# Performance work log

Measured on AMD Instinct MI355X. Metric: run time of the kernel, lower is better.

The kernel has to match this reference:

```python
import jax, jax.numpy as jnp
import numpy as np

G = 64          # graphs in batch
P = 31          # original nodes per graph
N_ORIG = G * P  # 1984 original nodes
N = N_ORIG + G  # 2048 total nodes (one virtual node per graph, appended at end)
D = 512         # hidden_dim
H = 8           # num_heads
DK = D // H     # per-head dim
FF = 2048       # dim_ff
L = 4           # num_layers
NF = 32         # num_node_features
MAX_SP = 100
MAX_DEG = 100


def setup_inputs() -> dict:
    key = jax.random.key(0)
    ks = jax.random.split(key, 24)
    s = 0.02
    return {
        "x": jax.random.normal(ks[0], (N_ORIG, NF), jnp.float32),
        "sp_matrix": jax.random.randint(ks[1], (N_ORIG, N_ORIG), 0, MAX_SP + 1, jnp.int32),
        "batch_ids": jnp.concatenate([
            jnp.repeat(jnp.arange(G, dtype=jnp.int32), P),
            jnp.arange(G, dtype=jnp.int32),
        ]),
        "degrees": jax.random.randint(ks[2], (N,), 0, MAX_DEG + 1, jnp.int32),
        "init_W": jax.random.normal(ks[3], (NF, D), jnp.float32) * s,
        "init_b": jnp.zeros((D,), jnp.float32),
        "cent_emb": jax.random.normal(ks[4], (MAX_DEG + 1, D), jnp.float32) * s,
        "dist_biases": jax.random.normal(ks[5], (MAX_SP + 2,), jnp.float32) * s,
        "virt_bias": jnp.zeros((), jnp.float32),
        "Wq": jax.random.normal(ks[6], (L, H, D, DK), jnp.float32) * s,
        "bq": jnp.zeros((L, H, DK), jnp.float32),
        "Wk": jax.random.normal(ks[7], (L, H, D, DK), jnp.float32) * s,
        "bk": jnp.zeros((L, H, DK), jnp.float32),
        "Wv": jax.random.normal(ks[8], (L, H, D, DK), jnp.float32) * s,
        "bv": jnp.zeros((L, H, DK), jnp.float32),
        "Wo": jax.random.normal(ks[9], (L, D, D), jnp.float32) * s,
        "bo": jnp.zeros((L, D), jnp.float32),
        "W1": jax.random.normal(ks[10], (L, D, FF), jnp.float32) * s,
        "b1": jnp.zeros((L, FF), jnp.float32),
        "W2": jax.random.normal(ks[11], (L, FF, D), jnp.float32) * s,
        "b2": jnp.zeros((L, D), jnp.float32),
    }


def _ln(h):
    # F.layer_norm with no affine params, eps=1e-5
    m = jnp.mean(h, axis=-1, keepdims=True)
    v = jnp.var(h, axis=-1, keepdims=True)
    return (h - m) / jnp.sqrt(v + 1e-5)


def reference(x, sp_matrix, batch_ids, degrees,
              init_W, init_b, cent_emb, dist_biases, virt_bias,
              Wq, bq, Wk, bk, Wv, bv, Wo, bo, W1, b1, W2, b2):
    same = batch_ids[:, None] == batch_ids[None, :]          # attention mask [N, N]
    is_virt = jnp.arange(N) >= N_ORIG

    # B matrix: fill with last distance bias (detached: torch uses .item()),
    # overwrite orig-orig block with sp-distance biases, virtual edges with
    # virt_bias, diagonal with dist_biases[0].
    fill = jax.lax.stop_gradient(dist_biases[-1])
    B = jnp.full((N, N), fill, dtype=jnp.float32)
    sp = jnp.minimum(sp_matrix, MAX_SP)
    B = B.at[:N_ORIG, :N_ORIG].set(dist_biases[sp])
    ve = (is_virt[:, None] ^ is_virt[None, :]) & same        # virt<->non-virt, same graph
    B = jnp.where(ve, virt_bias, B)
    diag = jnp.arange(N)
    B = B.at[diag, diag].set(dist_biases[0])

    # init projection, append virtual node states, add centrality encoding
    h = x @ init_W + init_b                                  # [N_ORIG, D]
    h = jnp.concatenate([h, jnp.zeros((G, D), h.dtype)], axis=0)   # [N, D]
    h = h + cent_emb[jnp.minimum(degrees, MAX_DEG)]

    scale = 1.0 / jnp.sqrt(jnp.float32(DK))
    for l in range(L):
        hn = _ln(h)
        Q = jnp.einsum('nd,hdk->hnk', hn, Wq[l]) + bq[l][:, None, :]   # [H, N, DK]
        K = jnp.einsum('nd,hdk->hnk', hn, Wk[l]) + bk[l][:, None, :]
        V = jnp.einsum('nd,hdk->hnk', hn, Wv[l]) + bv[l][:, None, :]
        logits = jnp.einsum('hik,hjk->hij', Q, K) * scale + B          # [H, N, N]
        logits = jnp.where(same, logits, -jnp.inf)
        w = jax.nn.softmax(logits, axis=-1)
        o = jnp.einsum('hij,hjk->hik', w, V)                           # [H, N, DK]
        o = jnp.transpose(o, (1, 0, 2)).reshape(N, D)                  # concat heads
        h = o @ Wo[l] + bo[l] + h                                      # residual
        hn2 = _ln(h)
        h = h + jax.nn.relu(hn2 @ W1[l] + b1[l]) @ W2[l] + b2[l]       # FFN residual

    return h[N_ORIG:]   # virtual node states, [G, D]
```

## Files before the change

kernel.cpp:

```cpp
#include <hip/hip_runtime.h>


#define NG   64
#define NP   31
#define NORI 1984
#define NT   2048
#define DIM  512
#define NHD  8
#define DKH  64
#define FFD  2048
#define NLAY 4
#define NFEA 32

typedef __attribute__((ext_vector_type(8))) short short8;
typedef __attribute__((ext_vector_type(4))) float floatx4;

__device__ __forceinline__ unsigned short f2bf(float f) {
    union { float f; unsigned u; } v; v.f = f;
    unsigned r = v.u + 0x7fffu + ((v.u >> 16) & 1u);
    return (unsigned short)(r >> 16);
}
__device__ __forceinline__ float bf2f(unsigned short u) {
    union { unsigned u; float f; } v; v.u = ((unsigned)u) << 16;
    return v.f;
}

__global__ __launch_bounds__(256) void build_B(
    const int* __restrict__ sp, const float* __restrict__ db,
    const float* __restrict__ virt_bias, float* __restrict__ Bg)
{
    int g = blockIdx.x;
    float vb = virt_bias[0];
    for (int e = threadIdx.x; e < 1024; e += 256) {
        int i = e >> 5, j = e & 31;
        float v;
        if (i == j) v = db[0];
        else if (i < NP && j < NP) {
            int s = sp[(size_t)(g * NP + i) * NORI + g * NP + j];
            v = db[s < 100 ? s : 100];
        } else v = vb;
        Bg[(size_t)g * 1024 + e] = v;
    }
}

__global__ __launch_bounds__(256) void init_h(
    const float* __restrict__ x, const int* __restrict__ degrees,
    const float* __restrict__ init_W, const float* __restrict__ init_b,
    const float* __restrict__ cent_emb, float* __restrict__ h)
{
    int n = blockIdx.x;
    int tid = threadIdx.x;
    __shared__ float xs[NFEA];
    if (n < NORI && tid < NFEA) xs[tid] = x[(size_t)n * NFEA + tid];
    __syncthreads();
    int deg = degrees[n]; if (deg > 100) deg = 100;
    for (int d = tid; d < DIM; d += 256) {
        float v = cent_emb[(size_t)deg * DIM + d];
        if (n < NORI) {
            float acc = init_b[d];
            #pragma unroll
            for (int k = 0; k < NFEA; ++k) acc += xs[k] * init_W[(size_t)k * DIM + d];
            v += acc;
        }
        h[(size_t)n * DIM + d] = v;
    }
}

__global__ __launch_bounds__(256) void qkv_prep(
    const float* __restrict__ Wq, const float* __restrict__ Wk, const float* __restrict__ Wv,
    unsigned short* __restrict__ Wt)
{
    int tile = blockIdx.x;
    int slice = tile >> 5;
    int tloc = tile & 31;
    int dt = tloc >> 1, kt = tloc & 1;
    int l = slice / 24; int rem = slice % 24; int which = rem >> 3; int hh = rem & 7;
    const float* W = (which == 0) ? Wq : (which == 1) ? Wk : Wv;
    const float* in = W + (size_t)(l * 8 + hh) * DIM * DKH;
    __shared__ float tl[32][33];
    int tr = threadIdx.x >> 5, tc = threadIdx.x & 31;
    #pragma unroll
    for (int p = 0; p < 4; ++p)
        tl[tr + p * 8][tc] = in[(size_t)(dt * 32 + tr + p * 8) * DKH + kt * 32 + tc];
    __syncthreads();
    unsigned short* out = Wt + ((size_t)l * 1536 + which * 512 + hh * 64 + kt * 32) * DIM + dt * 32;
    #pragma unroll
    for (int p = 0; p < 4; ++p)
        out[(size_t)(tr + p * 8) * DIM + tc] = f2bf(tl[tc][tr + p * 8]);
}

__global__ __launch_bounds__(256) void bias_prep(
    const float* __restrict__ bq, const float* __restrict__ bk, const float* __restrict__ bv,
    float* __restrict__ bqkv)
{
    int idx = blockIdx.x * 256 + threadIdx.x;
    if (idx >= NLAY * 1536) return;
    int l = idx / 1536, c = idx % 1536;
    int which = c >> 9, cc = c & 511;
    const float* b = (which == 0) ? bq : (which == 1) ? bk : bv;
    bqkv[idx] = b[(size_t)l * 512 + cc];
}

__global__ __launch_bounds__(256) void prep_w(
    const float* __restrict__ Wo, const float* __restrict__ W1, const float* __restrict__ W2,
    unsigned short* __restrict__ Wo_t, unsigned short* __restrict__ W1_t,
    unsigned short* __restrict__ W2_t)
{
    int id = blockIdx.x;
    const float* in; unsigned short* out; int R, C, l, rt, ct;
    if (id < 1024) {
        l = id >> 8; int t = id & 255; rt = t >> 4; ct = t & 15;
        in = Wo; out = Wo_t; R = 512; C = 512;
    } else if (id < 5120) {
        int t2 = id - 1024; l = t2 >> 10; int t = t2 & 1023; rt = t >> 6; ct = t & 63;
        in = W1; out = W1_t; R = 512; C = 2048;
    } else {
        int t2 = id - 5120; l = t2 >> 10; int t = t2 & 1023; rt = t >> 4; ct = t & 15;
        in = W2; out = W2_t; R = 2048; C = 512;
    }
    const float* ip = in + (size_t)l * R * C;
    unsigned short* op = out + (size_t)l * R * C;
    int r0 = rt * 32, c0 = ct * 32;
    __shared__ float tl[32][33];
    int tr = threadIdx.x >> 5, tc = threadIdx.x & 31;
    #pragma unroll
    for (int p = 0; p < 4; ++p)
        tl[tr + p * 8][tc] = ip[(size_t)(r0 + tr + p * 8) * C + c0 + tc];
    __syncthreads();
    #pragma unroll
    for (int p = 0; p < 4; ++p)
        op[(size_t)(c0 + tr + p * 8) * R + r0 + tc] = f2bf(tl[tc][tr + p * 8]);
}

__global__ __launch_bounds__(256) void layernorm_bf16(
    const float* __restrict__ in, unsigned short* __restrict__ out, int row0)
{
    int n = row0 + blockIdx.x;
    int tid = threadIdx.x;
    const float* row = in + (size_t)n * DIM;
    float v0 = row[tid], v1 = row[tid + 256];
    float s = v0 + v1;
    float sq = v0 * v0 + v1 * v1;
    #pragma unroll
    for (int off = 32; off > 0; off >>= 1) {
        s  += __shfl_down(s, off);
        sq += __shfl_down(sq, off);
    }
    __shared__ float red[8];
    int wave = tid >> 6;
    if ((tid & 63) == 0) { red[wave] = s; red[4 + wave] = sq; }
    __syncthreads();
    float ts  = red[0] + red[1] + red[2] + red[3];
    float tsq = red[4] + red[5] + red[6] + red[7];
    float m   = ts * (1.0f / DIM);
    float var = tsq * (1.0f / DIM) - m * m;
    float inv = rsqrtf(var + 1e-5f);
    out[(size_t)n * DIM + tid]       = f2bf((v0 - m) * inv);
    out[(size_t)n * DIM + tid + 256] = f2bf((v1 - m) * inv);
}

template<int SPLITK>
__global__ __launch_bounds__(256) void gemm_bf16(
    const unsigned short* __restrict__ A, const unsigned short* __restrict__ Bt,
    const float* __restrict__ bias, void* __restrict__ out,
    int Nfull, int K, int moff, int noff, int flags)
{
    __shared__ __align__(16) unsigned short Asl[64 * 72];
    __shared__ __align__(16) unsigned short Bsl[64 * 72];
    int tid = threadIdx.x;
    int row0 = moff + blockIdx.y * 64, col0 = noff + blockIdx.x * 64;
    if ((flags & 4) && col0 < 512 && row0 < NORI) return;
    int kslice = K / SPLITK;
    int kbeg = blockIdx.z * kslice;
    int wave = tid >> 6, lane = tid & 63;
    int quad = lane >> 4, m16 = lane & 15;
    int mw = (wave >> 1) * 32, nw = (wave & 1) * 32;
    floatx4 acc[2][2] = {};
    for (int k0 = kbeg; k0 < kbeg + kslice; k0 += 64) {
        #pragma unroll
        for (int p = 0; p < 2; ++p) {
            int idx = (p * 256 + tid) * 8;
            int r = idx >> 6, kk = idx & 63;
            *(float4*)(Asl + r * 72 + kk) =
                *(const float4*)(A + (size_t)(row0 + r) * K + k0 + kk);
            *(float4*)(Bsl + r * 72 + kk) =
                *(const float4*)(Bt + (size_t)(col0 + r) * K + k0 + kk);
        }
        __syncthreads();
        #pragma unroll
        for (int ks = 0; ks < 64; ks += 32) {
            short8 a[2], b[2];
            #pragma unroll
            for (int mi = 0; mi < 2; ++mi)
                a[mi] = *(const short8*)(Asl + (mw + mi * 16 + m16) * 72 + ks + quad * 8);
            #pragma unroll
            for (int ni = 0; ni < 2; ++ni)
                b[ni] = *(const short8*)(Bsl + (nw + ni * 16 + m16) * 72 + ks + quad * 8);
            #pragma unroll
            for (int mi = 0; mi < 2; ++mi)
                #pragma unroll
                for (int ni = 0; ni < 2; ++ni)
                    acc[mi][ni] = __builtin_amdgcn_mfma_f32_16x16x32_bf16(
                        a[mi], b[ni], acc[mi][ni], 0, 0, 0);
        }
        __syncthreads();
    }
    if (SPLITK == 1) {
        int do_relu = flags & 1, out_bf = flags & 2;
        #pragma unroll
        for (int mi = 0; mi < 2; ++mi) {
            #pragma unroll
            for (int ni = 0; ni < 2; ++ni) {
                int col = col0 + nw + ni * 16 + m16;
                float bval = bias ? bias[col] : 0.0f;
                #pragma unroll
                for (int rr = 0; rr < 4; ++rr) {
                    int row = row0 + mw + mi * 16 + quad * 4 + rr;
                    float v = acc[mi][ni][rr] + bval;
                    if (do_relu) v = fmaxf(v, 0.0f);
                    if (out_bf) ((unsigned short*)out)[(size_t)row * Nfull + col] = f2bf(v);
                    else        ((float*)out)[(size_t)row * Nfull + col] = v;
                }
            }
        }
    } else {
        float* o = (float*)out;
        float bscale = (blockIdx.z == 0) ? 1.0f : 0.0f;
        #pragma unroll
        for (int mi = 0; mi < 2; ++mi) {
            #pragma unroll
            for (int ni = 0; ni < 2; ++ni) {
                int col = col0 + nw + ni * 16 + m16;
                float bval = bias[col] * bscale;
                #pragma unroll
                for (int rr = 0; rr < 4; ++rr) {
                    int row = row0 + mw + mi * 16 + quad * 4 + rr;
                    atomicAdd(&o[(size_t)row * Nfull + col], acc[mi][ni][rr] + bval);
                }
            }
        }
    }
}

__global__ __launch_bounds__(256) void attention(
    const unsigned short* __restrict__ qkv,
    const float* __restrict__ Bg,
    unsigned short* __restrict__ O)
{
    int g = blockIdx.x >> 3;
    int hh = blockIdx.x & 7;
    __shared__ float Qs[32][65], Ks[32][65], Vs[32][65];
    __shared__ float S[32][33];
    int tid = threadIdx.x;
    int i = tid >> 3;
    int c0 = (tid & 7) * 8;
    int gn = (i < NP) ? g * NP + i : NORI + g;
    const unsigned short* base = qkv + (size_t)gn * 1536 + hh * DKH;
    short8 qv = *(const short8*)(base + c0);
    short8 kv = *(const short8*)(base + 512 + c0);
    short8 vv = *(const short8*)(base + 1024 + c0);
    #pragma unroll
    for (int j = 0; j < 8; ++j) {
        Qs[i][c0 + j] = bf2f((unsigned short)qv[j]);
        Ks[i][c0 + j] = bf2f((unsigned short)kv[j]);
        Vs[i][c0 + j] = bf2f((unsigned short)vv[j]);
    }
    __syncthreads();
    const float scale = 0.125f;
    #pragma unroll
    for (int e = 0; e < 4; ++e) {
        int idx = tid + e * 256;
        int si = idx >> 5, sj = idx & 31;
        float dot = 0.0f;
        #pragma unroll
        for (int k = 0; k < DKH; ++k) dot += Qs[si][k] * Ks[sj][k];
        S[si][sj] = dot * scale + Bg[(size_t)g * 1024 + si * 32 + sj];
    }
    __syncthreads();
    if (tid < 32) {
        float mx = -1e30f;
        #pragma unroll
        for (int j = 0; j < 32; ++j) mx = fmaxf(mx, S[tid][j]);
        float sum = 0.0f;
        #pragma unroll
        for (int j = 0; j < 32; ++j) { float e = __expf(S[tid][j] - mx); S[tid][j] = e; sum += e; }
        float inv = 1.0f / sum;
        #pragma unroll
        for (int j = 0; j < 32; ++j) S[tid][j] *= inv;
    }
    __syncthreads();
    short8 ov;
    #pragma unroll
    for (int cc = 0; cc < 8; ++cc) {
        float acc = 0.0f;
        #pragma unroll
        for (int j = 0; j < 32; ++j) acc += S[i][j] * Vs[j][c0 + cc];
        ov[cc] = (short)f2bf(acc);
    }
    *(short8*)(O + (size_t)gn * DIM + hh * DKH + c0) = ov;
}

__global__ __launch_bounds__(64) void attention_last(
    const unsigned short* __restrict__ qkv, const float* __restrict__ Bg,
    unsigned short* __restrict__ O)
{
    int g = blockIdx.x >> 3, hh = blockIdx.x & 7;
    __shared__ float Ks[32][65], Vs[32][65];
    __shared__ float Qs[64], P[32];
    int tid = threadIdx.x;
    int j = tid & 31, hf = tid >> 5;
    int gn = (j < NP) ? g * NP + j : NORI + g;
    const unsigned short* kb = qkv + (size_t)gn * 1536 + hh * DKH + 512 + hf * 32;
    #pragma unroll
    for (int c = 0; c < 32; c += 8) {
        short8 k8 = *(const short8*)(kb + c);
        short8 v8 = *(const short8*)(kb + 512 + c);
        #pragma unroll
        for (int t = 0; t < 8; ++t) {
            Ks[j][hf * 32 + c + t] = bf2f((unsigned short)k8[t]);
            Vs[j][hf * 32 + c + t] = bf2f((unsigned short)v8[t]);
        }
    }
    Qs[tid] = bf2f(qkv[(size_t)(NORI + g) * 1536 + hh * DKH + tid]);
    __syncthreads();
    float s;
    if (tid < 32) {
        float dot = 0.0f;
        #pragma unroll
        for (int k = 0; k < 64; ++k) dot += Qs[k] * Ks[tid][k];
        s = dot * 0.125f + Bg[(size_t)g * 1024 + 31 * 32 + tid];
    } else s = -1e30f;
    float mx = s;
    #pragma unroll
    for (int off = 32; off > 0; off >>= 1) mx = fmaxf(mx, __shfl_xor(mx, off));
    float e = (tid < 32) ? __expf(s - mx) : 0.0f;
    float sum = e;
    #pragma unroll
    for (int off = 32; off > 0; off >>= 1) sum += __shfl_xor(sum, off);
    if (tid < 32) P[tid] = e / sum;
    __syncthreads();
    float acc = 0.0f;
    #pragma unroll
    for (int jj = 0; jj < 32; ++jj) acc += P[jj] * Vs[jj][tid];
    O[(size_t)(NORI + g) * DIM + hh * DKH + tid] = f2bf(acc);
}

extern "C" void kernel_launch(void* const* d_in, const int* in_sizes, int n_in,
                              void* d_out, int out_size, void* d_ws, size_t ws_size,
                              hipStream_t stream)
{
    const float* x        = (const float*)d_in[0];
    const int*   sp       = (const int*)d_in[1];
    const int*   degrees  = (const int*)d_in[3];
    const float* init_W   = (const float*)d_in[4];
    const float* init_b   = (const float*)d_in[5];
    const float* cent_emb = (const float*)d_in[6];
    const float* db       = (const float*)d_in[7];
    const float* vbias    = (const float*)d_in[8];
    const float* Wq       = (const float*)d_in[9];
    const float* bq       = (const float*)d_in[10];
    const float* Wk       = (const float*)d_in[11];
    const float* bk       = (const float*)d_in[12];
    const float* Wv       = (const float*)d_in[13];
    const float* bv       = (const float*)d_in[14];
    const float* Wo       = (const float*)d_in[15];
    const float* bo       = (const float*)d_in[16];
    const float* W1       = (const float*)d_in[17];
    const float* b1       = (const float*)d_in[18];
    const float* W2       = (const float*)d_in[19];
    const float* b2       = (const float*)d_in[20];

    char* ws = (char*)d_ws;
    float*          h      = (float*)ws;          ws += (size_t)NT * DIM * 4;
    unsigned short* hn     = (unsigned short*)ws; ws += (size_t)NT * DIM * 2;
    unsigned short* o      = (unsigned short*)ws; ws += (size_t)NT * DIM * 2;
    unsigned short* qkv    = (unsigned short*)ws; ws += (size_t)NT * FFD * 2;
    float*          Bg     = (float*)ws;          ws += (size_t)NG * 1024 * 4;
    unsigned short* Wqkv_t = (unsigned short*)ws; ws += (size_t)NLAY * 1536 * DIM * 2;
    unsigned short* Wo_t   = (unsigned short*)ws; ws += (size_t)NLAY * DIM * DIM * 2;
    unsigned short* W1_t   = (unsigned short*)ws; ws += (size_t)NLAY * FFD * DIM * 2;
    unsigned short* W2_t   = (unsigned short*)ws; ws += (size_t)NLAY * DIM * FFD * 2;
    float*          bqkv   = (float*)ws;          ws += (size_t)NLAY * 1536 * 4;
    unsigned short* ffnb   = qkv;

    build_B<<<NG, 256, 0, stream>>>(sp, db, vbias, Bg);
    init_h<<<NT, 256, 0, stream>>>(x, degrees, init_W, init_b, cent_emb, h);
    qkv_prep<<<96 * 32, 256, 0, stream>>>(Wq, Wk, Wv, Wqkv_t);
    bias_prep<<<(NLAY * 1536 + 255) / 256, 256, 0, stream>>>(bq, bk, bv, bqkv);
    prep_w<<<9216, 256, 0, stream>>>(Wo, W1, W2, Wo_t, W1_t, W2_t);

    for (int l = 0; l < NLAY - 1; ++l) {
        layernorm_bf16<<<NT, 256, 0, stream>>>(h, hn, 0);
        gemm_bf16<1><<<dim3(1536 / 64, NT / 64), 256, 0, stream>>>(
            hn, Wqkv_t + (size_t)l * 1536 * DIM, bqkv + (size_t)l * 1536,
            qkv, 1536, DIM, 0, 0, 2);
        attention<<<NG * NHD, 256, 0, stream>>>(qkv, Bg, o);
        gemm_bf16<2><<<dim3(DIM / 64, NT / 64, 2), 256, 0, stream>>>(
            o, Wo_t + (size_t)l * DIM * DIM, bo + (size_t)l * DIM,
            h, DIM, DIM, 0, 0, 0);
        layernorm_bf16<<<NT, 256, 0, stream>>>(h, hn, 0);
        gemm_bf16<1><<<dim3(FFD / 64, NT / 64), 256, 0, stream>>>(
            hn, W1_t + (size_t)l * FFD * DIM, b1 + (size_t)l * FFD,
            ffnb, FFD, DIM, 0, 0, 3);
        gemm_bf16<4><<<dim3(DIM / 64, NT / 64, 4), 256, 0, stream>>>(
            ffnb, W2_t + (size_t)l * DIM * FFD, b2 + (size_t)l * DIM,
            h, DIM, FFD, 0, 0, 0);
    }

    {
        int l = NLAY - 1;
        layernorm_bf16<<<NT, 256, 0, stream>>>(h, hn, 0);
        gemm_bf16<1><<<dim3(1536 / 64, NT / 64), 256, 0, stream>>>(
            hn, Wqkv_t + (size_t)l * 1536 * DIM, bqkv + (size_t)l * 1536,
            qkv, 1536, DIM, 0, 0, 6);
        attention_last<<<NG * NHD, 64, 0, stream>>>(qkv, Bg, o);
        gemm_bf16<8><<<dim3(DIM / 64, 1, 8), 256, 0, stream>>>(
            o, Wo_t + (size_t)l * DIM * DIM, bo + (size_t)l * DIM,
            h, DIM, DIM, NORI, 0, 0);
        layernorm_bf16<<<NG, 256, 0, stream>>>(h, hn, NORI);
        gemm_bf16<1><<<dim3(FFD / 64, 1), 256, 0, stream>>>(
            hn, W1_t + (size_t)l * FFD * DIM, b1 + (size_t)l * FFD,
            ffnb, FFD, DIM, NORI, 0, 3);
        gemm_bf16<8><<<dim3(DIM / 64, 1, 8), 256, 0, stream>>>(
            ffnb, W2_t + (size_t)l * DIM * FFD, b2 + (size_t)l * DIM,
            h, DIM, FFD, NORI, 0, 0);
    }

    hipMemcpyAsync(d_out, h + (size_t)NORI * DIM, (size_t)NG * DIM * sizeof(float),
                   hipMemcpyDeviceToDevice, stream);
}
```

Measured before the change: 474.0 us.

## Add 128x128 tiled GEMM with direct global-to-LDS loads for full-size layers

Introduces a 128x128-tile GEMM kernel in which each wave computes a 64x64 sub-tile with 4x4 MFMA accumulators, and uses global_load_lds to copy operand tiles straight into unpadded shared memory. The full-batch QKV, Wo, W1 and W2 projections switch to it, and the Wo split-K rises to 4. The goal is more data reuse per loaded tile and fewer register round trips during staging. In exchange it raises register pressure, leaves the LDS unpadded (possible bank conflicts on the short8 reads), and launches fewer blocks, which lowers occupancy.

Measured after the change: 486.2 us. 1.03x slower.

```diff
diff --git a/kernel.cpp b/kernel.cpp
--- a/kernel.cpp
+++ b/kernel.cpp
@@ -14,6 +14,13 @@
 
 typedef __attribute__((ext_vector_type(8))) short short8;
 typedef __attribute__((ext_vector_type(4))) float floatx4;
+
+typedef __attribute__((address_space(3))) unsigned int lds_u32;
+typedef const __attribute__((address_space(1))) unsigned int glb_u32;
+
+__device__ __forceinline__ void gload16(const unsigned short* g, unsigned short* l) {
+    __builtin_amdgcn_global_load_lds((glb_u32*)g, (lds_u32*)l, 16, 0, 0);
+}
 
 __device__ __forceinline__ unsigned short f2bf(float f) {
     union { float f; unsigned u; } v; v.f = f;
@@ -160,16 +167,98 @@
 }
 
 template<int SPLITK>
-__global__ __launch_bounds__(256) void gemm_bf16(
+__global__ __launch_bounds__(256) void gemm128(
     const unsigned short* __restrict__ A, const unsigned short* __restrict__ Bt,
     const float* __restrict__ bias, void* __restrict__ out,
-    int Nfull, int K, int moff, int noff, int flags)
+    int Nfull, int K, int moff, int flags)
+{
+    __shared__ __align__(16) unsigned short Asl[128 * 64];
+    __shared__ __align__(16) unsigned short Bsl[128 * 64];
+    int tid = threadIdx.x;
+    int row0 = moff + blockIdx.y * 128, col0 = blockIdx.x * 128;
+    if ((flags & 4) && col0 < 512 && row0 + 128 <= NORI) return;
+    int kslice = K / SPLITK;
+    int kbeg = blockIdx.z * kslice;
+    int wave = tid >> 6, lane = tid & 63;
+    int quad = lane >> 4, m16 = lane & 15;
+    int mw = (wave >> 1) * 64, nw = (wave & 1) * 64;
+    int lrow = lane >> 3;
+    int lcol = (lane & 7) * 8;
+    floatx4 acc[4][4] = {};
+    for (int k0 = kbeg; k0 < kbeg + kslice; k0 += 64) {
+        #pragma unroll
+        for (int i = 0; i < 4; ++i) {
+            int seg = wave * 4 + i;
+            int r = seg * 8 + lrow;
+            gload16(A  + (size_t)(row0 + r) * K + k0 + lcol, Asl + seg * 512);
+            gload16(Bt + (size_t)(col0 + r) * K + k0 + lcol, Bsl + seg * 512);
+        }
+        __syncthreads();
+        #pragma unroll
+        for (int ks = 0; ks < 64; ks += 32) {
+            short8 a[4], b[4];
+            #pragma unroll
+            for (int mi = 0; mi < 4; ++mi)
+                a[mi] = *(const short8*)(Asl + (mw + mi * 16 + m16) * 64 + ks + quad * 8);
+            #pragma unroll
+            for (int ni = 0; ni < 4; ++ni)
+                b[ni] = *(const short8*)(Bsl + (nw + ni * 16 + m16) * 64 + ks + quad * 8);
+            #pragma unroll
+            for (int mi = 0; mi < 4; ++mi)
+                #pragma unroll
+                for (int ni = 0; ni < 4; ++ni)
+                    acc[mi][ni] = __builtin_amdgcn_mfma_f32_16x16x32_bf16(
+                        a[mi], b[ni], acc[mi][ni], 0, 0, 0);
+        }
+        __syncthreads();
+    }
+    if (SPLITK == 1) {
+        int do_relu = flags & 1, out_bf = flags & 2;
+        #pragma unroll
+        for (int mi = 0; mi < 4; ++mi) {
+            #pragma unroll
+            for (int ni = 0; ni < 4; ++ni) {
+                int col = col0 + nw + ni * 16 + m16;
+                float bval = bias[col];
+                #pragma unroll
+                for (int rr = 0; rr < 4; ++rr) {
+                    int row = row0 + mw + mi * 16 + quad * 4 + rr;
+                    float v = acc[mi][ni][rr] + bval;
+                    if (do_relu) v = fmaxf(v, 0.0f);
+                    if (out_bf) ((unsigned short*)out)[(size_t)row * Nfull + col] = f2bf(v);
+                    else        ((float*)out)[(size_t)row * Nfull + col] = v;
+                }
+            }
+        }
+    } else {
+        float* o = (float*)out;
+        float bscale = (blockIdx.z == 0) ? 1.0f : 0.0f;
+        #pragma unroll
+        for (int mi = 0; mi < 4; ++mi) {
+            #pragma unroll
+            for (int ni = 0; ni < 4; ++ni) {
+                int col = col0 + nw + ni * 16 + m16;
+                float bval = bias[col] * bscale;
+                #pragma unroll
+                for (int rr = 0; rr < 4; ++rr) {
+                    int row = row0 + mw + mi * 16 + quad * 4 + rr;
+                    atomicAdd(&o[(size_t)row * Nfull + col], acc[mi][ni][rr] + bval);
+                }
+            }
+        }
+    }
+}
+
+template<int SPLITK>
+__global__ __launch_bounds__(256) void gemm64(
+    const unsigned short* __restrict__ A, const unsigned short* __restrict__ Bt,
+    const float* __restrict__ bias, void* __restrict__ out,
+    int Nfull, int K, int moff, int flags)
 {
     __shared__ __align__(16) unsigned short Asl[64 * 72];
     __shared__ __align__(16) unsigned short Bsl[64 * 72];
     int tid = threadIdx.x;
-    int row0 = moff + blockIdx.y * 64, col0 = noff + blockIdx.x * 64;
-    if ((flags & 4) && col0 < 512 && row0 < NORI) return;
+    int row0 = moff + blockIdx.y * 64, col0 = blockIdx.x * 64;
     int kslice = K / SPLITK;
     int kbeg = blockIdx.z * kslice;
     int wave = tid >> 6, lane = tid & 63;
@@ -212,7 +301,7 @@
             #pragma unroll
             for (int ni = 0; ni < 2; ++ni) {
                 int col = col0 + nw + ni * 16 + m16;
-                float bval = bias ? bias[col] : 0.0f;
+                float bval = bias[col];
                 #pragma unroll
                 for (int rr = 0; rr < 4; ++rr) {
                     int row = row0 + mw + mi * 16 + quad * 4 + rr;
@@ -391,39 +480,39 @@
 
     for (int l = 0; l < NLAY - 1; ++l) {
         layernorm_bf16<<<NT, 256, 0, stream>>>(h, hn, 0);
-        gemm_bf16<1><<<dim3(1536 / 64, NT / 64), 256, 0, stream>>>(
+        gemm128<1><<<dim3(1536 / 128, NT / 128), 256, 0, stream>>>(
             hn, Wqkv_t + (size_t)l * 1536 * DIM, bqkv + (size_t)l * 1536,
-            qkv, 1536, DIM, 0, 0, 2);
+            qkv, 1536, DIM, 0, 2);
         attention<<<NG * NHD, 256, 0, stream>>>(qkv, Bg, o);
-        gemm_bf16<2><<<dim3(DIM / 64, NT / 64, 2), 256, 0, stream>>>(
+        gemm128<4><<<dim3(DIM / 128, NT / 128, 4), 256, 0, stream>>>(
             o, Wo_t + (size_t)l * DIM * DIM, bo + (size_t)l * DIM,
-            h, DIM, DIM, 0, 0, 0);
+            h, DIM, DIM, 0, 0);
         layernorm_bf16<<<NT, 256, 0, stream>>>(h, hn, 0);
-        gemm_bf16<1><<<dim3(FFD / 64, NT / 64), 256, 0, stream>>>(
+        gemm128<1><<<dim3(FFD / 128, NT / 128), 256, 0, stream>>>(
             hn, W1_t + (size_t)l * FFD * DIM, b1 + (size_t)l * FFD,
-            ffnb, FFD, DIM, 0, 0, 3);
-        gemm_bf16<4><<<dim3(DIM / 64, NT / 64, 4), 256, 0, stream>>>(
+            ffnb, FFD, DIM, 0, 3);
+        gemm128<4><<<dim3(DIM / 128, NT / 128, 4), 256, 0, stream>>>(
             ffnb, W2_t + (size_t)l * DIM * FFD, b2 + (size_t)l * DIM,
-            h, DIM, FFD, 0, 0, 0);
+            h, DIM, FFD, 0, 0);
     }
 
     {
         int l = NLAY - 1;
         layernorm_bf16<<<NT, 256, 0, stream>>>(h, hn, 0);
-        gemm_bf16<1><<<dim3(1536 / 64, NT / 64), 256, 0, stream>>>(
+        gemm128<1><<<dim3(1536 / 128, NT / 128), 256, 0, stream>>>(
             hn, Wqkv_t + (size_t)l * 1536 * DIM, bqkv + (size_t)l * 1536,
-            qkv, 1536, DIM, 0, 0, 6);
+            qkv, 1536, DIM, 0, 6);
         attention_last<<<NG * NHD, 64, 0, stream>>>(qkv, Bg, o);
-        gemm_bf16<8><<<dim3(DIM / 64, 1, 8), 256, 0, stream>>>(
+        gemm64<8><<<dim3(DIM / 64, 1, 8), 256, 0, stream>>>(
             o, Wo_t + (size_t)l * DIM * DIM, bo + (size_t)l * DIM,
-            h, DIM, DIM, NORI, 0, 0);
+            h, DIM, DIM, NORI, 0);
         layernorm_bf16<<<NG, 256, 0, stream>>>(h, hn, NORI);
-        gemm_bf16<1><<<dim3(FFD / 64, 1), 256, 0, stream>>>(
+        gemm64<1><<<dim3(FFD / 64, 1), 256, 0, stream>>>(
             hn, W1_t + (size_t)l * FFD * DIM, b1 + (size_t)l * FFD,
-            ffnb, FFD, DIM, NORI, 0, 3);
-        gemm_bf16<8><<<dim3(DIM / 64, 1, 8), 256, 0, stream>>>(
+            ffnb, FFD, DIM, NORI, 3);
+        gemm64<8><<<dim3(DIM / 64, 1, 8), 256, 0, stream>>>(
             ffnb, W2_t + (size_t)l * DIM * FFD, b2 + (size_t)l * DIM,
-            h, DIM, FFD, NORI, 0, 0);
+            h, DIM, FFD, NORI, 0);
     }
 
     hipMemcpyAsync(d_out, h + (size_t)NORI * DIM, (size_t)NG * DIM * sizeof(float),
```

## Remap GEMM blocks to XCDs and fold small prep kernels into others

Applied to the files above, without the earlier changes.

The GEMM kernel now takes a flat 1D grid and decodes its (row, col, k-slice) tile from the block id. Blocks that share the same row tile are placed on the same XCD, which is meant to improve L2 reuse of the A operand on the chiplet GPU. Separately, build_B is merged into init_h and bias_prep into qkv_prep, removing two kernel launches. The cost is extra index arithmetic per block, and the nullable-bias check is dropped.

Result: no change. 465.3 us (-1.8%).

```diff
diff --git a/kernel.cpp b/kernel.cpp
--- a/kernel.cpp
+++ b/kernel.cpp
@@ -25,31 +25,30 @@
     return v.f;
 }
 
-__global__ __launch_bounds__(256) void build_B(
-    const int* __restrict__ sp, const float* __restrict__ db,
-    const float* __restrict__ virt_bias, float* __restrict__ Bg)
-{
-    int g = blockIdx.x;
-    float vb = virt_bias[0];
-    for (int e = threadIdx.x; e < 1024; e += 256) {
-        int i = e >> 5, j = e & 31;
-        float v;
-        if (i == j) v = db[0];
-        else if (i < NP && j < NP) {
-            int s = sp[(size_t)(g * NP + i) * NORI + g * NP + j];
-            v = db[s < 100 ? s : 100];
-        } else v = vb;
-        Bg[(size_t)g * 1024 + e] = v;
-    }
-}
-
 __global__ __launch_bounds__(256) void init_h(
     const float* __restrict__ x, const int* __restrict__ degrees,
     const float* __restrict__ init_W, const float* __restrict__ init_b,
-    const float* __restrict__ cent_emb, float* __restrict__ h)
+    const float* __restrict__ cent_emb, float* __restrict__ h,
+    const int* __restrict__ sp, const float* __restrict__ db,
+    const float* __restrict__ virt_bias, float* __restrict__ Bg)
 {
     int n = blockIdx.x;
     int tid = threadIdx.x;
+    if (n >= NT) {
+        int g = n - NT;
+        float vb = virt_bias[0];
+        for (int e = tid; e < 1024; e += 256) {
+            int i = e >> 5, j = e & 31;
+            float v;
+            if (i == j) v = db[0];
+            else if (i < NP && j < NP) {
+                int s = sp[(size_t)(g * NP + i) * NORI + g * NP + j];
+                v = db[s < 100 ? s : 100];
+            } else v = vb;
+            Bg[(size_t)g * 1024 + e] = v;
+        }
+        return;
+    }
     __shared__ float xs[NFEA];
     if (n < NORI && tid < NFEA) xs[tid] = x[(size_t)n * NFEA + tid];
     __syncthreads();
@@ -68,9 +67,20 @@
 
 __global__ __launch_bounds__(256) void qkv_prep(
     const float* __restrict__ Wq, const float* __restrict__ Wk, const float* __restrict__ Wv,
-    unsigned short* __restrict__ Wt)
+    const float* __restrict__ bq, const float* __restrict__ bk, const float* __restrict__ bv,
+    unsigned short* __restrict__ Wt, float* __restrict__ bqkv)
 {
     int tile = blockIdx.x;
+    if (tile >= 3072) {
+        int idx = (tile - 3072) * 256 + threadIdx.x;
+        if (idx < NLAY * 1536) {
+            int l = idx / 1536, c = idx % 1536;
+            int which = c >> 9, cc = c & 511;
+            const float* b = (which == 0) ? bq : (which == 1) ? bk : bv;
+            bqkv[idx] = b[(size_t)l * 512 + cc];
+        }
+        return;
+    }
     int slice = tile >> 5;
     int tloc = tile & 31;
     int dt = tloc >> 1, kt = tloc & 1;
@@ -87,18 +97,6 @@
     #pragma unroll
     for (int p = 0; p < 4; ++p)
         out[(size_t)(tr + p * 8) * DIM + tc] = f2bf(tl[tc][tr + p * 8]);
-}
-
-__global__ __launch_bounds__(256) void bias_prep(
-    const float* __restrict__ bq, const float* __restrict__ bk, const float* __restrict__ bv,
-    float* __restrict__ bqkv)
-{
-    int idx = blockIdx.x * 256 + threadIdx.x;
-    if (idx >= NLAY * 1536) return;
-    int l = idx / 1536, c = idx % 1536;
-    int which = c >> 9, cc = c & 511;
-    const float* b = (which == 0) ? bq : (which == 1) ? bk : bv;
-    bqkv[idx] = b[(size_t)l * 512 + cc];
 }
 
 __global__ __launch_bounds__(256) void prep_w(
@@ -160,18 +158,29 @@
 }
 
 template<int SPLITK>
-__global__ __launch_bounds__(256) void gemm_bf16(
+__global__ __launch_bounds__(256) void gemm64(
     const unsigned short* __restrict__ A, const unsigned short* __restrict__ Bt,
     const float* __restrict__ bias, void* __restrict__ out,
-    int Nfull, int K, int moff, int noff, int flags)
+    int Nfull, int K, int moff, int flags, int P, int C)
 {
     __shared__ __align__(16) unsigned short Asl[64 * 72];
     __shared__ __align__(16) unsigned short Bsl[64 * 72];
+    int id = blockIdx.x;
+    int by, bx, bz;
+    if (P >= 8) {
+        int xcd = id & 7, t = id >> 3, G = P >> 3;
+        by = xcd + 8 * (t % G);
+        int r2 = t / G;
+        bx = r2 % C;
+        bz = r2 / C;
+    } else {
+        by = id % P; int r2 = id / P; bx = r2 % C; bz = r2 / C;
+    }
     int tid = threadIdx.x;
-    int row0 = moff + blockIdx.y * 64, col0 = noff + blockIdx.x * 64;
+    int row0 = moff + by * 64, col0 = bx * 64;
     if ((flags & 4) && col0 < 512 && row0 < NORI) return;
     int kslice = K / SPLITK;
-    int kbeg = blockIdx.z * kslice;
+    int kbeg = bz * kslice;
     int wave = tid >> 6, lane = tid & 63;
     int quad = lane >> 4, m16 = lane & 15;
     int mw = (wave >> 1) * 32, nw = (wave & 1) * 32;
@@ -212,7 +221,7 @@
             #pragma unroll
             for (int ni = 0; ni < 2; ++ni) {
                 int col = col0 + nw + ni * 16 + m16;
-                float bval = bias ? bias[col] : 0.0f;
+                float bval = bias[col];
                 #pragma unroll
                 for (int rr = 0; rr < 4; ++rr) {
                     int row = row0 + mw + mi * 16 + quad * 4 + rr;
@@ -225,7 +234,7 @@
         }
     } else {
         float* o = (float*)out;
-        float bscale = (blockIdx.z == 0) ? 1.0f : 0.0f;
+        float bscale = (bz == 0) ? 1.0f : 0.0f;
         #pragma unroll
         for (int mi = 0; mi < 2; ++mi) {
             #pragma unroll
@@ -383,47 +392,46 @@
     float*          bqkv   = (float*)ws;          ws += (size_t)NLAY * 1536 * 4;
     unsigned short* ffnb   = qkv;
 
-    build_B<<<NG, 256, 0, stream>>>(sp, db, vbias, Bg);
-    init_h<<<NT, 256, 0, stream>>>(x, degrees, init_W, init_b, cent_emb, h);
-    qkv_prep<<<96 * 32, 256, 0, stream>>>(Wq, Wk, Wv, Wqkv_t);
-    bias_prep<<<(NLAY * 1536 + 255) / 256, 256, 0, stream>>>(bq, bk, bv, bqkv);
+    init_h<<<NT + NG, 256, 0, stream>>>(x, degrees, init_W, init_b, cent_emb, h,
+                                        sp, db, vbias, Bg);
+    qkv_prep<<<3072 + 24, 256, 0, stream>>>(Wq, Wk, Wv, bq, bk, bv, Wqkv_t, bqkv);
     prep_w<<<9216, 256, 0, stream>>>(Wo, W1, W2, Wo_t, W1_t, W2_t);
 
     for (int l = 0; l < NLAY - 1; ++l) {
         layernorm_bf16<<<NT, 256, 0, stream>>>(h, hn, 0);
-        gemm_bf16<1><<<dim3(1536 / 64, NT / 64), 256, 0, stream>>>(
+        gemm64<1><<<32 * 24, 256, 0, stream>>>(
             hn, Wqkv_t + (size_t)l * 1536 * DIM, bqkv + (size_t)l * 1536,
-            qkv, 1536, DIM, 0, 0, 2);
+            qkv, 1536, DIM, 0, 2, 32, 24);
         attention<<<NG * NHD, 256, 0, stream>>>(qkv, Bg, o);
-        gemm_bf16<2><<<dim3(DIM / 64, NT / 64, 2), 256, 0, stream>>>(
+        gemm64<2><<<32 * 8 * 2, 256, 0, stream>>>(
             o, Wo_t + (size_t)l * DIM * DIM, bo + (size_t)l * DIM,
-            h, DIM, DIM, 0, 0, 0);
+            h, DIM, DIM, 0, 0, 32, 8);
         layernorm_bf16<<<NT, 256, 0, stream>>>(h, hn, 0);
-        gemm_bf16<1><<<dim3(FFD / 64, NT / 64), 256, 0, stream>>>(
+        gemm64<1><<<32 * 32, 256, 0, stream>>>(
             hn, W1_t + (size_t)l * FFD * DIM, b1 + (size_t)l * FFD,
-            ffnb, FFD, DIM, 0, 0, 3);
-        gemm_bf16<4><<<dim3(DIM / 64, NT / 64, 4), 256, 0, stream>>>(
+            ffnb, FFD, DIM, 0, 3, 32, 32);
+        gemm64<4><<<32 * 8 * 4, 256, 0, stream>>>(
             ffnb, W2_t + (size_t)l * DIM * FFD, b2 + (size_t)l * DIM,
-            h, DIM, FFD, 0, 0, 0);
+            h, DIM, FFD, 0, 0, 32, 8);
     }
 
     {
         int l = NLAY - 1;
         layernorm_bf16<<<NT, 256, 0, stream>>>(h, hn, 0);
-        gemm_bf16<1><<<dim3(1536 / 64, NT / 64), 256, 0, stream>>>(
+        gemm64<1><<<32 * 24, 256, 0, stream>>>(
             hn, Wqkv_t + (size_t)l * 1536 * DIM, bqkv + (size_t)l * 1536,
-            qkv, 1536, DIM, 0, 0, 6);
+            qkv, 1536, DIM, 0, 6, 32, 24);
         attention_last<<<NG * NHD, 64, 0, stream>>>(qkv, Bg, o);
-        gemm_bf16<8><<<dim3(DIM / 64, 1, 8), 256, 0, stream>>>(
+        gemm64<8><<<1 * 8 * 8, 256, 0, stream>>>(
             o, Wo_t + (size_t)l * DIM * DIM, bo + (size_t)l * DIM,
-            h, DIM, DIM, NORI, 0, 0);
+            h, DIM, DIM, NORI, 0, 1, 8);
         layernorm_bf16<<<NG, 256, 0, stream>>>(h, hn, NORI);
-        gemm_bf16<1><<<dim3(FFD / 64, 1), 256, 0, stream>>>(
+        gemm64<1><<<1 * 32, 256, 0, stream>>>(
             hn, W1_t + (size_t)l * FFD * DIM, b1 + (size_t)l * FFD,
-            ffnb, FFD, DIM, NORI, 0, 3);
-        gemm_bf16<8><<<dim3(DIM / 64, 1, 8), 256, 0, stream>>>(
+            ffnb, FFD, DIM, NORI, 3, 1, 32);
+        gemm64<8><<<1 * 8 * 8, 256, 0, stream>>>(
             ffnb, W2_t + (size_t)l * DIM * FFD, b2 + (size_t)l * DIM,
-            h, DIM, FFD, NORI, 0, 0);
+            h, DIM, FFD, NORI, 0, 1, 8);
     }
 
     hipMemcpyAsync(d_out, h + (size_t)NORI * DIM, (size_t)NG * DIM * sizeof(float),
```
